# Kernel optimization log

Hardware: AMD Instinct MI355X
Metric: run time of the kernel (lower is better)

The kernel has to match this reference:

```python
import jax, jax.numpy as jnp
import numpy as np
from jax import lax

B, T, V, E, H, L = 256, 512, 50000, 128, 256, 31
BN_EPS = 1e-5


def setup_inputs() -> dict:
    key = jax.random.key(0)
    ks = jax.random.split(key, 16)
    x = jax.random.randint(ks[0], (B, T), 0, V, dtype=jnp.int64 if jax.config.jax_enable_x64 else jnp.int32)
    lengths = jnp.sort(jax.random.randint(ks[1], (B,), T // 2, T + 1))[::-1]
    s = 0.05
    return {
        'x': x,
        'lengths': lengths,
        'embed_table': jax.random.normal(ks[2], (V, E), jnp.float32) * s,
        'conv1_w': jax.random.normal(ks[3], (E, E, 3), jnp.float32) * s,
        'conv1_b': jax.random.normal(ks[4], (E,), jnp.float32) * s,
        'conv2_w': jax.random.normal(ks[5], (E, E, 5), jnp.float32) * s,
        'conv2_b': jax.random.normal(ks[6], (E,), jnp.float32) * s,
        'bn_gamma': jnp.ones((2 * E,), jnp.float32),
        'bn_beta': jnp.zeros((2 * E,), jnp.float32),
        'w_ih': jax.random.normal(ks[7], (4 * H, 2 * E), jnp.float32) * s,
        'w_hh': jax.random.normal(ks[8], (4 * H, H), jnp.float32) * s,
        'b_ih': jax.random.normal(ks[9], (4 * H,), jnp.float32) * s,
        'b_hh': jax.random.normal(ks[10], (4 * H,), jnp.float32) * s,
        'lin_w': jax.random.normal(ks[11], (L, H), jnp.float32) * s,
        'lin_b': jax.random.normal(ks[12], (L,), jnp.float32) * s,
    }


def _conv1d(x, w, b, pad):
    # x: (B,C,T), w: (O,I,K)
    y = lax.conv_general_dilated(x, w, window_strides=(1,), padding=[(pad, pad)],
                                 dimension_numbers=('NCH', 'OIH', 'NCH'))
    return y + b[None, :, None]


def reference(x, lengths, embed_table, conv1_w, conv1_b, conv2_w, conv2_b,
              bn_gamma, bn_beta, w_ih, w_hh, b_ih, b_hh, lin_w, lin_b):
    emb = embed_table[x]                      # (B,T,E)
    xc = jnp.transpose(emb, (0, 2, 1))        # (B,E,T)
    embeddings = jnp.concatenate([_conv1d(xc, conv1_w, conv1_b, 1),
                                  _conv1d(xc, conv2_w, conv2_b, 2)], axis=1)  # (B,2E,T)

    # BatchNorm1d in training mode: batch stats over (B,T) per channel (biased var)
    mean = embeddings.mean(axis=(0, 2))
    var = embeddings.var(axis=(0, 2))
    scale = (bn_gamma * lax.rsqrt(var + BN_EPS))[None, :, None]
    act = jax.nn.relu((embeddings - mean[None, :, None]) * scale + bn_beta[None, :, None])

    # single-layer LSTM over packed (length-masked) sequence; PyTorch gate order i,f,g,o
    seq = jnp.transpose(act, (2, 0, 1))       # (T,B,2E)
    h0 = jnp.zeros((B, H), act.dtype)
    c0 = jnp.zeros((B, H), act.dtype)
    ts = jnp.arange(T)

    def step(carry, inp):
        h, c = carry
        x_t, t = inp
        g = x_t @ w_ih.T + b_ih + h @ w_hh.T + b_hh        # (B,4H)
        i, f, gg, o = jnp.split(g, 4, axis=-1)
        c_new = jax.nn.sigmoid(f) * c + jax.nn.sigmoid(i) * jnp.tanh(gg)
        h_new = jax.nn.sigmoid(o) * jnp.tanh(c_new)
        m = (t < lengths)[:, None]
        return (jnp.where(m, h_new, h), jnp.where(m, c_new, c)), None

    (hn, _), _ = lax.scan(step, (h0, c0), (seq, ts))

    # vectorized form of the per-timestep diagonal-matmul attention loop
    attn = jnp.einsum('bct,bc->bt', embeddings, hn) / (256.0 ** 0.5)  # (B,T)
    attn_out = jnp.einsum('bt,bct->bc', attn, embeddings)            # (B,2E)

    logits = hn @ lin_w.T + lin_b
    return logits, attn_out
```

## Files before the change

kernel.cpp:

```cpp
#include <hip/hip_runtime.h>
#include <stdint.h>


typedef __bf16 bf16x8 __attribute__((ext_vector_type(8)));
typedef float  f32x4  __attribute__((ext_vector_type(4)));
typedef int    i32x8  __attribute__((ext_vector_type(8)));

__device__ __forceinline__ float bf2f(uint16_t h){
  union { uint32_t u; float f; } v; v.u = ((uint32_t)h) << 16; return v.f;
}
__device__ __forceinline__ uint16_t f2bf(float f){
  union { float f; uint32_t u; } v; v.f = f;
  return (uint16_t)((v.u + 0x7FFFu + ((v.u >> 16) & 1u)) >> 16);
}
__device__ __forceinline__ bf16x8 ld_frag(const uint16_t* p){
  union { int4 i; bf16x8 b; } u; u.i = *(const int4*)p; return u.b;
}
__device__ __forceinline__ f32x4 mfma16(bf16x8 a, bf16x8 b, f32x4 c){
  return __builtin_amdgcn_mfma_f32_16x16x32_bf16(a, b, c, 0, 0, 0);
}
__device__ __forceinline__ float sigm(float x){
  return __builtin_amdgcn_rcpf(1.f + __expf(-x));
}
__device__ __forceinline__ float tanh_(float x){
  return 2.f * __builtin_amdgcn_rcpf(1.f + __expf(-2.f * x)) - 1.f;
}

#define MFMA_MX(a, b, c, sa, sb) \
  __builtin_amdgcn_mfma_scale_f32_16x16x128_f8f6f4((a), (b), (c), 0, 0, 0, (sa), 0, (sb))

__device__ __forceinline__ void dma16(const void* g, void* l){
  __builtin_amdgcn_global_load_lds(
      (const __attribute__((address_space(1))) uint32_t*)g,
      (__attribute__((address_space(3))) uint32_t*)l, 16, 0, 0);
}
__device__ __forceinline__ void emit2(uint8_t* bH, uint8_t* bL, int off, float h){
  float h16 = h * 16.f;
  int p1 = __builtin_amdgcn_cvt_pk_fp8_f32(h16, h16, 0, false);
  float dec = __builtin_amdgcn_cvt_f32_fp8(p1, 0);
  float r16 = (h16 - dec) * 16.f;
  int p2 = __builtin_amdgcn_cvt_pk_fp8_f32(r16, r16, 0, false);
  bH[off] = (uint8_t)(p1 & 0xff);
  bL[off] = (uint8_t)(p2 & 0xff);
}

__global__ __launch_bounds__(256) void k_sniff(const uint32_t* __restrict__ e,
                                               int* __restrict__ flag)
{
  __shared__ int cnt;
  int tid = threadIdx.x;
  if (tid == 0) cnt = 0;
  __syncthreads();
  uint32_t u = e[tid];
  uint32_t ex = (u >> 7) & 0xFFu;
  if (ex >= 0x60u && ex <= 0x7Eu) atomicAdd(&cnt, 1);
  __syncthreads();
  if (tid == 0) flag[0] = (cnt >= 192) ? 1 : 0;
}

struct CvtDesc { const void* s; uint16_t* d; int n; int c0; };
struct CvtArgs { CvtDesc a[13]; };

__global__ __launch_bounds__(256) void k_cvt(CvtArgs A, const int* __restrict__ flag)
{
  int ch = blockIdx.x;
  int i = 0;
  #pragma unroll
  for (int k = 1; k < 13; ++k) if (ch >= A.a[k].c0) i = k;
  const void* s = A.a[i].s;
  uint16_t*   d = A.a[i].d;
  int n = A.a[i].n;
  int base = (ch - A.a[i].c0) * 4096 + threadIdx.x;
  int isb = *flag;
  #pragma unroll 4
  for (int r = 0; r < 16; ++r) {
    int idx = base + r * 256;
    if (idx < n)
      d[idx] = isb ? ((const uint16_t*)s)[idx] : f2bf(((const float*)s)[idx]);
  }
}

__global__ __launch_bounds__(256) void k_prep(
    const uint16_t* __restrict__ c1w, const uint16_t* __restrict__ c2w,
    const uint16_t* __restrict__ wih, const uint16_t* __restrict__ whh,
    uint16_t* __restrict__ fragC, uint16_t* __restrict__ fragI,
    uint2* __restrict__ fragH8, float* __restrict__ bnbuf,
    float* __restrict__ wsHf, float* __restrict__ wsC)
{
  int g = blockIdx.x * 256 + threadIdx.x;
  if (g < 20480) {
    int tile = g >> 6, lane = g & 63;
    int kt = tile >> 4, nt = tile & 15;
    int q = lane >> 4, c16 = lane & 15;
    int dlt = kt >> 2;
    int o = nt * 16 + c16;
    union { int4 i; uint16_t u[8]; } v;
    #pragma unroll
    for (int j = 0; j < 8; ++j) {
      int i = (kt & 3) * 32 + q * 8 + j;
      uint16_t val = 0;
      if (o < 128) { int k = dlt - 1; if (k >= 0 && k < 3) val = c1w[(o*128 + i)*3 + k]; }
      else         { int k = dlt;     if (k < 5)           val = c2w[((o-128)*128 + i)*5 + k]; }
      v.u[j] = val;
    }
    *(int4*)(fragC + tile * 512 + lane * 8) = v.i;
  } else if (g < 53248) {
    int gg = g - 20480;
    int tile = gg >> 6, lane = gg & 63;
    int nt = tile >> 3, kt = tile & 7;
    int q = lane >> 4, c16 = lane & 15;
    *(int4*)(fragI + tile * 512 + lane * 8) =
        *(const int4*)(wih + (nt*16 + c16)*256 + kt*32 + q*8);
  } else if (g < 86016) {
    int gg = g - 53248;
    int item = gg >> 2, part = gg & 3;
    int tile = item >> 6, lane = item & 63;
    int nt = tile >> 1, kb = tile & 1;
    int q = lane >> 4, c16 = lane & 15;
    const uint16_t* src = whh + (nt*16 + c16)*256 + kb*128 + q*32 + part*8;
    float f[8];
    #pragma unroll
    for (int j = 0; j < 8; ++j) f[j] = bf2f(src[j]) * 16.f;
    int lo = __builtin_amdgcn_cvt_pk_fp8_f32(f[0], f[1], 0, false);
    lo     = __builtin_amdgcn_cvt_pk_fp8_f32(f[2], f[3], lo, true);
    int hi = __builtin_amdgcn_cvt_pk_fp8_f32(f[4], f[5], 0, false);
    hi     = __builtin_amdgcn_cvt_pk_fp8_f32(f[6], f[7], hi, true);
    fragH8[(tile*64 + lane)*4 + part] = make_uint2((uint32_t)lo, (uint32_t)hi);
  } else if (g < 102400) {
    ((int4*)wsHf)[g - 86016] = make_int4(0,0,0,0);
  } else if (g < 118784) {
    ((int4*)wsC)[g - 102400] = make_int4(0,0,0,0);
  } else if (g < 118912) {
    ((int4*)bnbuf)[g - 118784] = make_int4(0,0,0,0);
  }
}

__global__ __launch_bounds__(256) void k_conv(
    const int* __restrict__ x, const uint16_t* __restrict__ etab,
    const uint16_t* __restrict__ fragC,
    const uint16_t* __restrict__ c1b, const uint16_t* __restrict__ c2b,
    uint16_t* __restrict__ y, float* __restrict__ bnbuf)
{
  __shared__ __align__(16) uint16_t embS[68 * 136];
  int blk = blockIdx.x;
  int b = blk >> 3, t0 = (blk & 7) * 64;
  int tid = threadIdx.x;
  int lane = tid & 63, w = tid >> 6;
  int q = lane >> 4, c16 = lane & 15;

  for (int s = tid; s < 1088; s += 256) {
    int r = s >> 4, seg = s & 15;
    int t = t0 - 2 + r;
    int4 val = make_int4(0,0,0,0);
    if (t >= 0 && t < 512) {
      int idx = x[b*512 + t];
      val = *(const int4*)(etab + (size_t)idx*128 + seg*8);
    }
    *(int4*)(embS + r*136 + seg*8) = val;
  }
  __syncthreads();

  f32x4 acc[4][4];
  #pragma unroll
  for (int i = 0; i < 4; ++i)
    #pragma unroll
    for (int j = 0; j < 4; ++j) acc[i][j] = (f32x4){0.f,0.f,0.f,0.f};

  #pragma unroll 4
  for (int kt = 0; kt < 20; ++kt) {
    int dlt = kt >> 2;
    int i0 = (kt & 3)*32 + q*8;
    bf16x8 a[4];
    #pragma unroll
    for (int Mt = 0; Mt < 4; ++Mt)
      a[Mt] = ld_frag(embS + (Mt*16 + c16 + dlt)*136 + i0);
    #pragma unroll
    for (int ntl = 0; ntl < 4; ++ntl) {
      int nt = w*4 + ntl;
      bf16x8 bf = ld_frag(fragC + (kt*16 + nt)*512 + lane*8);
      #pragma unroll
      for (int Mt = 0; Mt < 4; ++Mt)
        acc[ntl][Mt] = mfma16(a[Mt], bf, acc[ntl][Mt]);
    }
  }

  #pragma unroll
  for (int ntl = 0; ntl < 4; ++ntl) {
    int ch = (w*4 + ntl)*16 + c16;
    float bias = bf2f(ch < 128 ? c1b[ch] : c2b[ch - 128]);
    float s0 = 0.f, s1 = 0.f;
    #pragma unroll
    for (int Mt = 0; Mt < 4; ++Mt) {
      #pragma unroll
      for (int r = 0; r < 4; ++r) {
        float v = acc[ntl][Mt][r] + bias;
        int t = t0 + Mt*16 + q*4 + r;
        y[((size_t)b*512 + t)*256 + ch] = f2bf(v);
        s0 += v; s1 += v*v;
      }
    }
    s0 += __shfl_xor(s0, 16); s0 += __shfl_xor(s0, 32);
    s1 += __shfl_xor(s1, 16); s1 += __shfl_xor(s1, 32);
    if (q == 0) { atomicAdd(&bnbuf[ch], s0); atomicAdd(&bnbuf[256 + ch], s1); }
  }
}

__global__ void k_bn(const uint16_t* __restrict__ gamma,
                     const uint16_t* __restrict__ beta,
                     float* __restrict__ bnbuf)
{
  int c = threadIdx.x;
  const float inv = 1.f / 131072.f;
  float mean = bnbuf[c] * inv;
  float var  = fmaxf(bnbuf[256 + c] * inv - mean*mean, 0.f);
  float sc   = bf2f(gamma[c]) * rsqrtf(var + 1e-5f);
  bnbuf[512 + c] = sc;
  bnbuf[768 + c] = bf2f(beta[c]) - mean * sc;
}

__global__ __launch_bounds__(256) void k_gx(
    const uint16_t* __restrict__ y, const float* __restrict__ bnbuf,
    const uint16_t* __restrict__ fragI, const uint16_t* __restrict__ bih,
    const uint16_t* __restrict__ bhh, uint16_t* __restrict__ gx, int tbase)
{
  __shared__ __align__(16) uint16_t aS[16384];
  int Mblk = blockIdx.x, Nblk = blockIdx.y;
  int tl = Mblk >> 2;
  int b0 = (Mblk & 3) * 64;
  int t = tbase + tl;
  int tid = threadIdx.x, lane = tid & 63, w = tid >> 6;
  int q = lane >> 4, c16 = lane & 15;

  for (int s = tid; s < 2048; s += 256) {
    int row = s >> 5, seg = s & 31;
    union { int4 i; uint16_t u[8]; } vv, oo;
    vv.i = *(const int4*)(y + ((size_t)(b0 + row)*512 + t)*256 + seg*8);
    #pragma unroll
    for (int j = 0; j < 8; ++j) {
      int ch = seg*8 + j;
      float f = bf2f(vv.u[j]) * bnbuf[512 + ch] + bnbuf[768 + ch];
      oo.u[j] = f2bf(fmaxf(f, 0.f));
    }
    int Mt = row >> 4, mL = row & 15, kt2 = seg >> 2, qq = seg & 3;
    *(int4*)(aS + ((Mt*8 + kt2)*64 + qq*16 + mL)*8) = oo.i;
  }
  __syncthreads();

  f32x4 acc[4][4];
  #pragma unroll
  for (int ntl = 0; ntl < 4; ++ntl) {
    int n = (Nblk*16 + w*4 + ntl)*16 + c16;
    float bias = bf2f(bih[n]) + bf2f(bhh[n]);
    #pragma unroll
    for (int Mt = 0; Mt < 4; ++Mt) acc[ntl][Mt] = (f32x4){bias,bias,bias,bias};
  }
  #pragma unroll
  for (int kt = 0; kt < 8; ++kt) {
    bf16x8 a[4];
    #pragma unroll
    for (int Mt = 0; Mt < 4; ++Mt)
      a[Mt] = ld_frag(aS + ((Mt*8 + kt)*64 + lane)*8);
    #pragma unroll
    for (int ntl = 0; ntl < 4; ++ntl) {
      int nt = Nblk*16 + w*4 + ntl;
      bf16x8 bf = ld_frag(fragI + ((size_t)(nt*8 + kt))*512 + lane*8);
      #pragma unroll
      for (int Mt = 0; Mt < 4; ++Mt)
        acc[ntl][Mt] = mfma16(a[Mt], bf, acc[ntl][Mt]);
    }
  }
  #pragma unroll
  for (int ntl = 0; ntl < 4; ++ntl) {
    int nt = Nblk*16 + w*4 + ntl;
    #pragma unroll
    for (int Mt = 0; Mt < 4; ++Mt) {
      int b4 = (Mblk & 3)*16 + Mt*4 + q;
      uint32_t lo = (uint32_t)f2bf(acc[ntl][Mt][0]) | ((uint32_t)f2bf(acc[ntl][Mt][1]) << 16);
      uint32_t hi = (uint32_t)f2bf(acc[ntl][Mt][2]) | ((uint32_t)f2bf(acc[ntl][Mt][3]) << 16);
      uint2 vv = {lo, hi};
      *(uint2*)(gx + ((size_t)(tl*64 + b4))*4096 + (nt*16 + c16)*4) = vv;
    }
  }
}

__global__ __launch_bounds__(512, 2) void k_lstm(
    const uint16_t* __restrict__ gx, const uint2* __restrict__ fragH8,
    const int* __restrict__ lengths, float* __restrict__ wsHf,
    float* __restrict__ wsC, float* __restrict__ hn,
    int tbase, int tcount, int last)
{
  __shared__ __align__(16) uint8_t hH[2][4096];
  __shared__ __align__(16) uint8_t hL[2][4096];
  __shared__ __align__(16) uint8_t gxS[2][8192];
  __shared__ __align__(16) float   scr[8][512];

  int b4 = blockIdx.x;
  int tid = threadIdx.x, lane = tid & 63, w = tid >> 6;
  int q = lane >> 4, c16 = lane & 15;
  int row = b4*4 + q;

  int li    = lengths[row];
  int Tmax  = lengths[b4*4];
  int liMin = lengths[b4*4 + 3];

  int ntg[8];
  i32x8 breg[8][2];
  #pragma unroll
  for (int gp = 0; gp < 8; ++gp) {
    ntg[gp] = (gp >> 1)*16 + 2*w + (gp & 1);
    #pragma unroll
    for (int kb = 0; kb < 2; ++kb) {
      const int4* s4 = (const int4*)&fragH8[((ntg[gp]*2 + kb)*64 + lane)*4];
      union { int4 i[2]; i32x8 v; } u;
      u.i[0] = s4[0]; u.i[1] = s4[1];
      breg[gp][kb] = u.v;
    }
  }

  int up[2], off2[2];
  #pragma unroll
  for (int p = 0; p < 2; ++p) {
    int u = 32*w + p*16 + c16;
    up[p] = u;
    off2[p] = ((u >> 5)*16 + q)*32 + (u & 31);
  }

  float cr[2], hr[2];
  #pragma unroll
  for (int p = 0; p < 2; ++p) {
    cr[p] = wsC [row*256 + up[p]];
    hr[p] = wsHf[row*256 + up[p]];
  }

  ((int4*)hH)[tid] = make_int4(0,0,0,0);
  ((int4*)hL)[tid] = make_int4(0,0,0,0);
  __syncthreads();
  #pragma unroll
  for (int p = 0; p < 2; ++p)
    emit2(&hH[0][0], &hL[0][0], off2[p], hr[p]);

  dma16((const uint8_t*)(gx + (size_t)b4*4096) + tid*16, &gxS[0][tid*16]);
  __syncthreads();

  int cur = 0;
  int tEnd = min(tbase + tcount, Tmax);

  for (int t = tbase; t < tEnd; ++t) {
    {
      int tn = (t + 1 < tEnd) ? (t + 1 - tbase) : (t - tbase);
      dma16((const uint8_t*)(gx + ((size_t)(tn*64 + b4))*4096) + tid*16,
            &gxS[cur ^ 1][tid*16]);
    }

    f32x4 acc[8];
    #pragma unroll
    for (int gp = 0; gp < 8; ++gp) {
      uint2 gg = *(const uint2*)(&gxS[cur][(ntg[gp]*16 + c16)*8]);
      acc[gp][0] = bf2f((uint16_t)(gg.x & 0xffffu));
      acc[gp][1] = bf2f((uint16_t)(gg.x >> 16));
      acc[gp][2] = bf2f((uint16_t)(gg.y & 0xffffu));
      acc[gp][3] = bf2f((uint16_t)(gg.y >> 16));
    }

    #pragma unroll
    for (int kb = 0; kb < 2; ++kb) {
      int ao = ((kb*4 + q)*16 + c16)*32;
      union { int4 i[2]; i32x8 v; } aH, aL;
      aH.i[0] = *(const int4*)&hH[cur][ao];
      aH.i[1] = *(const int4*)&hH[cur][ao + 16];
      aL.i[0] = *(const int4*)&hL[cur][ao];
      aL.i[1] = *(const int4*)&hL[cur][ao + 16];
      #pragma unroll
      for (int gp = 0; gp < 8; ++gp) {
        acc[gp] = MFMA_MX(aH.v, breg[gp][kb], acc[gp], 0x7B7B7B7B, 0x7B7B7B7B);
        acc[gp] = MFMA_MX(aL.v, breg[gp][kb], acc[gp], 0x77777777, 0x7B7B7B7B);
      }
    }

    if (q == 0) {
      #pragma unroll
      for (int gp = 0; gp < 8; ++gp) {
        int p = gp & 1, gd = gp >> 1;
        #pragma unroll
        for (int r = 0; r < 4; ++r)
          scr[w][((r*2 + p)*16 + c16)*4 + gd] = acc[gp][r];
      }
    }
    __builtin_amdgcn_wave_barrier();
    asm volatile("s_waitcnt lgkmcnt(0)" ::: "memory");

    #pragma unroll
    for (int p = 0; p < 2; ++p) {
      f32x4 gv = *(const f32x4*)(&scr[w][((q*2 + p)*16 + c16)*4]);
      float cn = sigm(gv[1])*cr[p] + sigm(gv[0])*tanh_(gv[2]);
      float hw = sigm(gv[3])*tanh_(cn);
      if (t >= liMin) {
        bool upd = (t < li);
        cn = upd ? cn : cr[p];
        hw = upd ? hw : hr[p];
      }
      cr[p] = cn; hr[p] = hw;
      emit2(&hH[cur ^ 1][0], &hL[cur ^ 1][0], off2[p], hw);
    }

    __syncthreads();
    cur ^= 1;
  }

  #pragma unroll
  for (int p = 0; p < 2; ++p) {
    wsC [row*256 + up[p]] = cr[p];
    wsHf[row*256 + up[p]] = hr[p];
  }
  if (last) {
    #pragma unroll
    for (int p = 0; p < 2; ++p)
      hn[row*256 + up[p]] = hr[p];
  }
}

__global__ __launch_bounds__(256) void k_attn(
    const uint16_t* __restrict__ y, const float* __restrict__ hn,
    const uint16_t* __restrict__ linw, const uint16_t* __restrict__ linb,
    void* __restrict__ outv, const int* __restrict__ flag)
{
  __shared__ float hnS[256];
  __shared__ float attnS[512];
  int b = blockIdx.x;
  int tid = threadIdx.x, lane = tid & 63, w = tid >> 6;
  int isb = *flag;
  hnS[tid] = hn[b*256 + tid];
  __syncthreads();
  for (int t = w; t < 512; t += 4) {
    uint2 d = *(const uint2*)(y + ((size_t)b*512 + t)*256 + lane*4);
    float s = bf2f((uint16_t)(d.x & 0xffffu)) * hnS[lane*4 + 0]
            + bf2f((uint16_t)(d.x >> 16))     * hnS[lane*4 + 1]
            + bf2f((uint16_t)(d.y & 0xffffu)) * hnS[lane*4 + 2]
            + bf2f((uint16_t)(d.y >> 16))     * hnS[lane*4 + 3];
    #pragma unroll
    for (int off = 32; off >= 1; off >>= 1) s += __shfl_xor(s, off);
    if (lane == 0) attnS[t] = s * 0.0625f;
  }
  __syncthreads();
  float acc = 0.f;
  #pragma unroll 4
  for (int t = 0; t < 512; ++t)
    acc += attnS[t] * bf2f(y[((size_t)b*512 + t)*256 + tid]);
  if (isb) ((uint16_t*)outv)[7936 + b*256 + tid] = f2bf(acc);
  else     ((float*)outv)[7936 + b*256 + tid] = acc;
  if (tid < 31) {
    float a2 = bf2f(linb[tid]);
    for (int k = 0; k < 256; ++k) a2 += hnS[k] * bf2f(linw[tid*256 + k]);
    if (isb) ((uint16_t*)outv)[b*31 + tid] = f2bf(a2);
    else     ((float*)outv)[b*31 + tid] = a2;
  }
}

extern "C" void kernel_launch(void* const* d_in, const int* in_sizes, int n_in,
                              void* d_out, int out_size, void* d_ws, size_t ws_size,
                              hipStream_t stream)
{
  (void)in_sizes; (void)out_size;
  if (n_in < 15) return;
  const int* x   = (const int*)d_in[0];
  const int* len = (const int*)d_in[1];

  uint8_t* p = (uint8_t*)d_ws;
  auto take = [&](size_t n){ uint8_t* r = p; p += (n + 255) & ~(size_t)255; return r; };
  int*      flag  = (int*)take(256);
  uint16_t* c1bC  = (uint16_t*)take(256);
  uint16_t* c2bC  = (uint16_t*)take(256);
  uint16_t* bngC  = (uint16_t*)take(512);
  uint16_t* bnbC  = (uint16_t*)take(512);
  uint16_t* bihC  = (uint16_t*)take(2048);
  uint16_t* bhhC  = (uint16_t*)take(2048);
  uint16_t* linwC = (uint16_t*)take(15872);
  uint16_t* linbC = (uint16_t*)take(64);
  uint16_t* fragC = (uint16_t*)take(327680);
  uint16_t* fragI = (uint16_t*)take(524288);
  uint2*    fragH8= (uint2*)take(262144);
  float*    bnbuf = (float*)take(4096);
  float*    wsHf  = (float*)take(262144);
  float*    wsC   = (float*)take(262144);
  float*    hnbuf = (float*)take(262144);
  uint16_t* y     = (uint16_t*)take(67108864ull);
  uint16_t* gxb   = (uint16_t*)take(67108864ull);
  if ((size_t)(p - (uint8_t*)d_ws) > ws_size) return;

  uint16_t* etabC = gxb;
  uint16_t* c1wC  = (uint16_t*)((uint8_t*)gxb + 16u*1024*1024);
  uint16_t* c2wC  = (uint16_t*)((uint8_t*)gxb + 17u*1024*1024);
  uint16_t* wihC  = (uint16_t*)((uint8_t*)gxb + 18u*1024*1024);
  uint16_t* whhC  = (uint16_t*)((uint8_t*)gxb + 19u*1024*1024);

  k_sniff<<<1, 256, 0, stream>>>((const uint32_t*)d_in[2], flag);

  CvtArgs A;
  int c0 = 0;
  auto put = [&](int i, const void* s, uint16_t* d, int n){
    A.a[i].s = s; A.a[i].d = d; A.a[i].n = n; A.a[i].c0 = c0;
    c0 += (n + 4095) / 4096;
  };
  put(0,  d_in[2],  etabC, 6400000);
  put(1,  d_in[3],  c1wC,  49152);
  put(2,  d_in[4],  c1bC,  128);
  put(3,  d_in[5],  c2wC,  81920);
  put(4,  d_in[6],  c2bC,  128);
  put(5,  d_in[7],  bngC,  256);
  put(6,  d_in[8],  bnbC,  256);
  put(7,  d_in[9],  wihC,  262144);
  put(8,  d_in[10], whhC,  262144);
  put(9,  d_in[11], bihC,  1024);
  put(10, d_in[12], bhhC,  1024);
  put(11, d_in[13], linwC, 7936);
  put(12, d_in[14], linbC, 31);
  k_cvt<<<c0, 256, 0, stream>>>(A, flag);

  k_prep<<<512, 256, 0, stream>>>(c1wC, c2wC, wihC, whhC, fragC, fragI, fragH8,
                                  bnbuf, wsHf, wsC);
  k_conv<<<2048, 256, 0, stream>>>(x, etabC, fragC, c1bC, c2bC, y, bnbuf);
  k_bn<<<1, 256, 0, stream>>>(bngC, bnbC, bnbuf);
  for (int c = 0; c < 4; ++c) {
    k_gx<<<dim3(512, 4), 256, 0, stream>>>(y, bnbuf, fragI, bihC, bhhC, gxb, c*128);
    k_lstm<<<64, 512, 0, stream>>>(gxb, fragH8, len, wsHf, wsC, hnbuf,
                                   c*128, 128, (c == 3) ? 1 : 0);
  }
  k_attn<<<256, 256, 0, stream>>>(y, hnbuf, linwC, linbC, d_out, flag);
}
```

Before: 1.482 ms.

## Run one LSTM block per batch row instead of per four-row group

The recurrent LSTM kernel now launches 256 blocks, one per batch row, instead of 64 blocks that each handle four rows. Only the first quarter-wave row of the MFMA output is used. Gate math happens directly in registers, which drops the LDS scratch transpose and the per-row length masking, and each block stops at its own sequence length. This spreads the serial recurrence over more CUs and shortens per-step latency, but it wastes three quarters of the MFMA rows and has each block reload its own weight fragments.

```diff
diff --git a/kernel.cpp b/kernel.cpp
--- a/kernel.cpp
+++ b/kernel.cpp
@@ -289,19 +289,15 @@
     float* __restrict__ wsC, float* __restrict__ hn,
     int tbase, int tcount, int last)
 {
-  __shared__ __align__(16) uint8_t hH[2][4096];
-  __shared__ __align__(16) uint8_t hL[2][4096];
+  __shared__ __align__(16) uint8_t hP[2][2][4096];
   __shared__ __align__(16) uint8_t gxS[2][8192];
-  __shared__ __align__(16) float   scr[8][512];
-
-  int b4 = blockIdx.x;
+
+  int row = blockIdx.x;
   int tid = threadIdx.x, lane = tid & 63, w = tid >> 6;
   int q = lane >> 4, c16 = lane & 15;
-  int row = b4*4 + q;
-
-  int li    = lengths[row];
-  int Tmax  = lengths[b4*4];
-  int liMin = lengths[b4*4 + 3];
+
+  int li   = lengths[row];
+  int b4g  = row >> 2, rloc = row & 3;
 
   int ntg[8];
   i32x8 breg[8][2];
@@ -322,54 +318,51 @@
   for (int p = 0; p < 2; ++p) {
     int u = 32*w + p*16 + c16;
     up[p] = u;
-    off2[p] = ((u >> 5)*16 + q)*32 + (u & 31);
-  }
-
-  float cr[2], hr[2];
-  #pragma unroll
-  for (int p = 0; p < 2; ++p) {
-    cr[p] = wsC [row*256 + up[p]];
-    hr[p] = wsHf[row*256 + up[p]];
-  }
-
-  ((int4*)hH)[tid] = make_int4(0,0,0,0);
-  ((int4*)hL)[tid] = make_int4(0,0,0,0);
-  __syncthreads();
-  #pragma unroll
-  for (int p = 0; p < 2; ++p)
-    emit2(&hH[0][0], &hL[0][0], off2[p], hr[p]);
-
-  dma16((const uint8_t*)(gx + (size_t)b4*4096) + tid*16, &gxS[0][tid*16]);
+    off2[p] = (u >> 5)*512 + (u & 31);
+  }
+
+  float cr[2] = {0.f, 0.f}, hr[2] = {0.f, 0.f};
+  if (q == 0) {
+    #pragma unroll
+    for (int p = 0; p < 2; ++p) {
+      cr[p] = wsC [row*256 + up[p]];
+      hr[p] = wsHf[row*256 + up[p]];
+    }
+  }
+
+  ((int4*)hP)[tid]       = make_int4(0,0,0,0);
+  ((int4*)hP)[tid + 512] = make_int4(0,0,0,0);
+  __syncthreads();
+  if (q == 0) {
+    #pragma unroll
+    for (int p = 0; p < 2; ++p)
+      emit2(&hP[0][0][0], &hP[0][1][0], off2[p], hr[p]);
+  }
+  dma16((const uint8_t*)(gx + (size_t)b4g*4096) + tid*16, &gxS[0][tid*16]);
   __syncthreads();
 
   int cur = 0;
-  int tEnd = min(tbase + tcount, Tmax);
+  int tEnd = min(tbase + tcount, li);
 
   for (int t = tbase; t < tEnd; ++t) {
     {
       int tn = (t + 1 < tEnd) ? (t + 1 - tbase) : (t - tbase);
-      dma16((const uint8_t*)(gx + ((size_t)(tn*64 + b4))*4096) + tid*16,
+      dma16((const uint8_t*)(gx + ((size_t)(tn*64 + b4g))*4096) + tid*16,
             &gxS[cur ^ 1][tid*16]);
     }
 
     f32x4 acc[8];
     #pragma unroll
-    for (int gp = 0; gp < 8; ++gp) {
-      uint2 gg = *(const uint2*)(&gxS[cur][(ntg[gp]*16 + c16)*8]);
-      acc[gp][0] = bf2f((uint16_t)(gg.x & 0xffffu));
-      acc[gp][1] = bf2f((uint16_t)(gg.x >> 16));
-      acc[gp][2] = bf2f((uint16_t)(gg.y & 0xffffu));
-      acc[gp][3] = bf2f((uint16_t)(gg.y >> 16));
-    }
+    for (int gp = 0; gp < 8; ++gp) acc[gp] = (f32x4){0.f,0.f,0.f,0.f};
 
     #pragma unroll
     for (int kb = 0; kb < 2; ++kb) {
       int ao = ((kb*4 + q)*16 + c16)*32;
       union { int4 i[2]; i32x8 v; } aH, aL;
-      aH.i[0] = *(const int4*)&hH[cur][ao];
-      aH.i[1] = *(const int4*)&hH[cur][ao + 16];
-      aL.i[0] = *(const int4*)&hL[cur][ao];
-      aL.i[1] = *(const int4*)&hL[cur][ao + 16];
+      aH.i[0] = *(const int4*)&hP[cur][0][ao];
+      aH.i[1] = *(const int4*)&hP[cur][0][ao + 16];
+      aL.i[0] = *(const int4*)&hP[cur][1][ao];
+      aL.i[1] = *(const int4*)&hP[cur][1][ao + 16];
       #pragma unroll
       for (int gp = 0; gp < 8; ++gp) {
         acc[gp] = MFMA_MX(aH.v, breg[gp][kb], acc[gp], 0x7B7B7B7B, 0x7B7B7B7B);
@@ -378,44 +371,34 @@
     }
 
     if (q == 0) {
-      #pragma unroll
-      for (int gp = 0; gp < 8; ++gp) {
-        int p = gp & 1, gd = gp >> 1;
-        #pragma unroll
-        for (int r = 0; r < 4; ++r)
-          scr[w][((r*2 + p)*16 + c16)*4 + gd] = acc[gp][r];
+      const uint16_t* gs = (const uint16_t*)&gxS[cur][0];
+      float pre[8];
+      #pragma unroll
+      for (int gp = 0; gp < 8; ++gp)
+        pre[gp] = acc[gp][0] + bf2f(gs[(ntg[gp]*16 + c16)*4 + rloc]);
+      #pragma unroll
+      for (int p = 0; p < 2; ++p) {
+        float cn = sigm(pre[2 + p])*cr[p] + sigm(pre[0 + p])*tanh_(pre[4 + p]);
+        float hw = sigm(pre[6 + p])*tanh_(cn);
+        cr[p] = cn; hr[p] = hw;
+        emit2(&hP[cur ^ 1][0][0], &hP[cur ^ 1][1][0], off2[p], hw);
       }
     }
-    __builtin_amdgcn_wave_barrier();
-    asm volatile("s_waitcnt lgkmcnt(0)" ::: "memory");
-
-    #pragma unroll
-    for (int p = 0; p < 2; ++p) {
-      f32x4 gv = *(const f32x4*)(&scr[w][((q*2 + p)*16 + c16)*4]);
-      float cn = sigm(gv[1])*cr[p] + sigm(gv[0])*tanh_(gv[2]);
-      float hw = sigm(gv[3])*tanh_(cn);
-      if (t >= liMin) {
-        bool upd = (t < li);
-        cn = upd ? cn : cr[p];
-        hw = upd ? hw : hr[p];
-      }
-      cr[p] = cn; hr[p] = hw;
-      emit2(&hH[cur ^ 1][0], &hL[cur ^ 1][0], off2[p], hw);
-    }
-
     __syncthreads();
     cur ^= 1;
   }
 
-  #pragma unroll
-  for (int p = 0; p < 2; ++p) {
-    wsC [row*256 + up[p]] = cr[p];
-    wsHf[row*256 + up[p]] = hr[p];
-  }
-  if (last) {
-    #pragma unroll
-    for (int p = 0; p < 2; ++p)
-      hn[row*256 + up[p]] = hr[p];
+  if (q == 0) {
+    #pragma unroll
+    for (int p = 0; p < 2; ++p) {
+      wsC [row*256 + up[p]] = cr[p];
+      wsHf[row*256 + up[p]] = hr[p];
+    }
+    if (last) {
+      #pragma unroll
+      for (int p = 0; p < 2; ++p)
+        hn[row*256 + up[p]] = hr[p];
+    }
   }
 }
 
@@ -522,8 +505,8 @@
   k_bn<<<1, 256, 0, stream>>>(bngC, bnbC, bnbuf);
   for (int c = 0; c < 4; ++c) {
     k_gx<<<dim3(512, 4), 256, 0, stream>>>(y, bnbuf, fragI, bihC, bhhC, gxb, c*128);
-    k_lstm<<<64, 512, 0, stream>>>(gxb, fragH8, len, wsHf, wsC, hnbuf,
-                                   c*128, 128, (c == 3) ? 1 : 0);
+    k_lstm<<<256, 512, 0, stream>>>(gxb, fragH8, len, wsHf, wsC, hnbuf,
+                                    c*128, 128, (c == 3) ? 1 : 0);
   }
   k_attn<<<256, 256, 0, stream>>>(y, hnbuf, linwC, linbC, d_out, flag);
 }
```

New measurement: 1.239 ms. 1.2x faster.
